# Optimization experiments

Hardware: AMD Instinct MI355X
Metric: run time of the kernel (lower is better)

The kernel has to match this reference:

```python
import jax, jax.numpy as jnp
import numpy as np

P = 2_000_000   # total gathered points (N1+N2+... after pillar grouping)
C_IN = 10       # mlps[0]: point feats + pillar-center offsets
C_OUT = 64      # mlps[1]
M = 200_000     # number of non-empty pillars (pillar_indices.shape[0])
BN_EPS = 1e-3


def setup_inputs() -> dict:
    key = jax.random.key(0)
    k0, k1, k2, k3, k4 = jax.random.split(key, 5)
    return {
        "group_features": jax.random.normal(k0, (P, C_IN), dtype=jnp.float32),
        "pillar_set_indices": jax.random.randint(k1, (P,), 0, M, dtype=jnp.int32),
        "num_pillars": M,
        # Linear(bias=False) weight, xavier-ish scale; stored (C_IN, C_OUT) so fwd is x @ W
        "W": jax.random.normal(k2, (C_IN, C_OUT), dtype=jnp.float32) * np.float32(1.0 / np.sqrt(C_IN)),
        "gamma": jnp.ones((C_OUT,), dtype=jnp.float32),
        "beta": jnp.zeros((C_OUT,), dtype=jnp.float32),
        "running_mean": jax.random.normal(k3, (C_OUT,), dtype=jnp.float32) * 0.1,
        "running_var": jax.random.uniform(k4, (C_OUT,), dtype=jnp.float32, minval=0.5, maxval=1.5),
    }


def reference(group_features, pillar_set_indices, num_pillars, W, gamma, beta, running_mean, running_var):
    # shared MLP: Linear(bias=False) -> BatchNorm1d(eval, eps=1e-3) -> ReLU
    h = group_features @ W                                   # (P, C_OUT)
    inv_std = gamma * jax.lax.rsqrt(running_var + BN_EPS)    # fold BN scale
    h = jax.nn.relu(h * inv_std + (beta - running_mean * inv_std))
    # scatter_max segment pooling into pillars; empty pillars -> 0 (ReLU output >= 0)
    pooled = jax.ops.segment_max(h, pillar_set_indices, num_segments=num_pillars)
    pillar_features = jnp.maximum(pooled, jnp.float32(0.0))  # (M, C_OUT)
    return pillar_features
```

## Files before the change

### kernel.cpp

```cpp
#include <hip/hip_runtime.h>


#define C_IN   10
#define C_OUT  64
#define BSHIFT 7
#define BPILL  128
#define MAXNBP 2048
#define NREG   8
#define SBLK   256
#define SCHUNK 2048
#define PPT    (SCHUNK / SBLK)
#define PBLK   512
#define SENT   (128u << 24)

typedef _Float16 half8 __attribute__((ext_vector_type(8)));
typedef float    f32x4 __attribute__((ext_vector_type(4)));

__global__ __launch_bounds__(SBLK)
void k_hist(const int* __restrict__ idx, int* __restrict__ tots,
            int P, int NBpad) {
    __shared__ int lh[MAXNBP];
    const int t = threadIdx.x;
    for (int b = t; b < NBpad; b += SBLK) lh[b] = 0;
    __syncthreads();
    const int base = blockIdx.x * SCHUNK;
#pragma unroll
    for (int i = 0; i < PPT; ++i) {
        int p = base + i * SBLK + t;
        if (p < P) atomicAdd(&lh[idx[p] >> BSHIFT], 1);
    }
    __syncthreads();
    int* row = tots + (size_t)(blockIdx.x & (NREG - 1)) * NBpad;
    for (int b = t; b < NBpad; b += SBLK) {
        int h = lh[b];
        if (h) atomicAdd(&row[b], h);
    }
}

__global__ __launch_bounds__(256)
void k_scan(const int* __restrict__ tots, int* __restrict__ starts,
            int* __restrict__ cursor, int E) {
    __shared__ int tmp[256];
    const int t = threadIdx.x;
    const int C = (E + 255) / 256;
    int my = 0;
    for (int j = 0; j < C; ++j) {
        int e = t * C + j;
        if (e < E) my += (tots[e] + 15) & ~15;
    }
    tmp[t] = my; __syncthreads();
#pragma unroll
    for (int off = 1; off < 256; off <<= 1) {
        int x = (t >= off) ? tmp[t - off] : 0;
        __syncthreads(); tmp[t] += x; __syncthreads();
    }
    int ex = tmp[t] - my;
    for (int j = 0; j < C; ++j) {
        int e = t * C + j;
        if (e < E) {
            starts[e] = ex; cursor[e] = ex;
            ex += (tots[e] + 15) & ~15;
        }
    }
    if (t == 255) starts[E] = ex;
}

__global__ __launch_bounds__(256)
void k_padfill(const int* __restrict__ tots, const int* __restrict__ starts,
               unsigned int* __restrict__ sorted, int E) {
    int e = blockIdx.x * 256 + threadIdx.x;
    if (e >= E) return;
    int s = starts[e] + tots[e];
    int e1 = starts[e + 1];
    for (int i = s; i < e1; ++i) sorted[i] = SENT;
}

__global__ __launch_bounds__(SBLK)
void k_split(const int* __restrict__ idx, int* __restrict__ cursor,
             unsigned int* __restrict__ sorted, int P, int NBpad) {
    __shared__ int lh[MAXNBP];
    __shared__ int rbase[MAXNBP];
    const int t = threadIdx.x;
    for (int b = t; b < NBpad; b += SBLK) lh[b] = 0;
    __syncthreads();
    const int base = blockIdx.x * SCHUNK;
    int mm[PPT];
#pragma unroll
    for (int i = 0; i < PPT; ++i) {
        int p = base + i * SBLK + t;
        mm[i] = (p < P) ? idx[p] : -1;
        if (mm[i] >= 0) atomicAdd(&lh[mm[i] >> BSHIFT], 1);
    }
    __syncthreads();
    int* crow = cursor + (size_t)(blockIdx.x & (NREG - 1)) * NBpad;
    for (int b = t; b < NBpad; b += SBLK) {
        int h = lh[b];
        rbase[b] = h ? atomicAdd(&crow[b], h) : 0;
        lh[b] = 0;
    }
    __syncthreads();
#pragma unroll
    for (int i = 0; i < PPT; ++i) {
        if (mm[i] >= 0) {
            int p = base + i * SBLK + t;
            int b = mm[i] >> BSHIFT;
            int slot = rbase[b] + atomicAdd(&lh[b], 1);
            sorted[slot] = (unsigned)p | ((unsigned)(mm[i] & (BPILL - 1)) << 24);
        }
    }
}

__global__ __launch_bounds__(PBLK, 8)
void k_pool(const float* __restrict__ gf,
            const unsigned int* __restrict__ sorted,
            const int* __restrict__ starts,
            const float* __restrict__ W,
            const float* __restrict__ gamma,
            const float* __restrict__ beta,
            const float* __restrict__ rmean,
            const float* __restrict__ rvar,
            float* __restrict__ out, int M, int NBpad) {
    __shared__ unsigned int acc[129 * 65];
    const int t = threadIdx.x;
    const int lane = t & 63;
    const int wv = t >> 6;
    const int n = lane & 15;
    const int q = lane >> 4;

    for (int i = t; i < 129 * 65; i += PBLK) acc[i] = 0u;

    half8 bfrag[4];
    float inv[4], bia[4];
#pragma unroll
    for (int tt = 0; tt < 4; ++tt) {
        int c = tt * 16 + n;
#pragma unroll
        for (int j = 0; j < 8; ++j) {
            int k = q * 8 + j;
            bfrag[tt][j] = (k < C_IN) ? (_Float16)W[k * C_OUT + c] : (_Float16)0.f;
        }
        float is = gamma[c] * rsqrtf(rvar[c] + 1e-3f);
        inv[tt] = is;
        bia[tt] = fmaf(-rmean[c], is, beta[c]);
    }
    __syncthreads();

    const int e  = wv * NBpad + blockIdx.x;
    const int s0 = starts[e];
    const int s1 = starts[e + 1];
    const float2* gf2 = (const float2*)gf;

    for (int rb = s0; rb < s1; rb += 64) {
        unsigned v = (rb + lane < s1) ? sorted[rb + lane] : SENT;
        const float2* src = gf2 + (size_t)(v & 0xFFFFFFu) * 5;
        float2 x0 = src[0], x1 = src[1], x2 = src[2], x3 = src[3], x4 = src[4];
        int u0 = __builtin_bit_cast(int, __builtin_amdgcn_cvt_pkrtz(x0.x, x0.y));
        int u1 = __builtin_bit_cast(int, __builtin_amdgcn_cvt_pkrtz(x1.x, x1.y));
        int u2 = __builtin_bit_cast(int, __builtin_amdgcn_cvt_pkrtz(x2.x, x2.y));
        int u3 = __builtin_bit_cast(int, __builtin_amdgcn_cvt_pkrtz(x3.x, x3.y));
        int u4 = __builtin_bit_cast(int, __builtin_amdgcn_cvt_pkrtz(x4.x, x4.y));

        const int ng = min(4, (s1 - rb) >> 4);
#pragma unroll
        for (int g = 0; g < 4; ++g) {
            if (g >= ng) break;
            const int sl = (g << 4) + n;
            int b0 = __shfl(u0, sl, 64);
            int b1 = __shfl(u1, sl, 64);
            int b2 = __shfl(u2, sl, 64);
            int b3 = __shfl(u3, sl, 64);
            int b4 = __shfl(u4, sl, 64);
            int4 a32;
            a32.x = (q == 0) ? b0 : ((q == 1) ? b4 : 0);
            a32.y = (q == 0) ? b1 : 0;
            a32.z = (q == 0) ? b2 : 0;
            a32.w = (q == 0) ? b3 : 0;
            half8 a = __builtin_bit_cast(half8, a32);
            f32x4 z = {0.f, 0.f, 0.f, 0.f};
            f32x4 d0 = __builtin_amdgcn_mfma_f32_16x16x32_f16(a, bfrag[0], z, 0, 0, 0);
            f32x4 d1 = __builtin_amdgcn_mfma_f32_16x16x32_f16(a, bfrag[1], z, 0, 0, 0);
            f32x4 d2 = __builtin_amdgcn_mfma_f32_16x16x32_f16(a, bfrag[2], z, 0, 0, 0);
            f32x4 d3 = __builtin_amdgcn_mfma_f32_16x16x32_f16(a, bfrag[3], z, 0, 0, 0);
#pragma unroll
            for (int r = 0; r < 4; ++r) {
                int pv = __shfl((int)v, (g << 4) + (q << 2) + r, 64);
                int abase = (int)(((unsigned)pv) >> 24) * 65 + n;
                float h0 = fmaxf(fmaf(d0[r], inv[0], bia[0]), 0.f);
                float h1 = fmaxf(fmaf(d1[r], inv[1], bia[1]), 0.f);
                float h2 = fmaxf(fmaf(d2[r], inv[2], bia[2]), 0.f);
                float h3 = fmaxf(fmaf(d3[r], inv[3], bia[3]), 0.f);
                atomicMax(&acc[abase +  0], __float_as_uint(h0));
                atomicMax(&acc[abase + 16], __float_as_uint(h1));
                atomicMax(&acc[abase + 32], __float_as_uint(h2));
                atomicMax(&acc[abase + 48], __float_as_uint(h3));
            }
        }
    }
    __syncthreads();

    const int mbase = blockIdx.x * BPILL;
#pragma unroll
    for (int i = 0; i < (BPILL * C_OUT) / PBLK; ++i) {
        int wdx = i * PBLK + t;
        int row = wdx >> 6, c = wdx & 63;
        int m = mbase + row;
        if (m < M) out[(size_t)m * C_OUT + c] = __uint_as_float(acc[row * 65 + c]);
    }
}

extern "C" void kernel_launch(void* const* d_in, const int* in_sizes, int n_in,
                              void* d_out, int out_size, void* d_ws, size_t ws_size,
                              hipStream_t stream) {
    const float* gf    = (const float*)d_in[0];
    const int*   idx   = (const int*)  d_in[1];
    const float* W     = (const float*)d_in[3];
    const float* gamma = (const float*)d_in[4];
    const float* beta  = (const float*)d_in[5];
    const float* rmean = (const float*)d_in[6];
    const float* rvar  = (const float*)d_in[7];
    float*       out   = (float*)d_out;

    const int P  = in_sizes[0] / C_IN;
    const int M  = out_size / C_OUT;
    const int NB    = (M + BPILL - 1) >> BSHIFT;
    const int NBpad = (NB + 32) & ~31;
    const int E     = NREG * NBpad;
    const int NSB   = (P + SCHUNK - 1) / SCHUNK;

    char* ws = (char*)d_ws;
    auto align256 = [](size_t x) { return (x + 255) & ~(size_t)255; };
    int* tots   = (int*)ws;  ws += align256((size_t)E * 4);
    int* starts = (int*)ws;  ws += align256((size_t)(E + 1) * 4);
    int* cursor = (int*)ws;  ws += align256((size_t)E * 4);
    unsigned int* sorted = (unsigned int*)ws;

    hipMemsetAsync(tots, 0, (size_t)E * 4, stream);
    k_hist   <<<NSB, SBLK, 0, stream>>>(idx, tots, P, NBpad);
    k_scan   <<<1,   256, 0, stream>>>(tots, starts, cursor, E);
    k_padfill<<<(E + 255) / 256, 256, 0, stream>>>(tots, starts, sorted, E);
    k_split  <<<NSB, SBLK, 0, stream>>>(idx, cursor, sorted, P, NBpad);
    k_pool   <<<NB,  PBLK, 0, stream>>>(gf, sorted, starts, W, gamma, beta,
                                        rmean, rvar, out, M, NBpad);
}
```

Measured before the change: 261.9 us.

## Fuse histogram, scan and scatter into one cooperative kernel; double-buffer pool loads

```diff
diff --git a/kernel.cpp b/kernel.cpp
--- a/kernel.cpp
+++ b/kernel.cpp
@@ -1,4 +1,5 @@
 #include <hip/hip_runtime.h>
+#include <hip/hip_cooperative_groups.h>
 
 
 #define C_IN   10
@@ -8,7 +9,7 @@
 #define MAXNBP 2048
 #define NREG   8
 #define SBLK   256
-#define SCHUNK 2048
+#define SCHUNK 4096
 #define PPT    (SCHUNK / SBLK)
 #define PBLK   512
 #define SENT   (128u << 24)
@@ -16,33 +17,40 @@
 typedef _Float16 half8 __attribute__((ext_vector_type(8)));
 typedef float    f32x4 __attribute__((ext_vector_type(4)));
 
-__global__ __launch_bounds__(SBLK)
-void k_hist(const int* __restrict__ idx, int* __restrict__ tots,
-            int P, int NBpad) {
+namespace cg = cooperative_groups;
+
+__global__ __launch_bounds__(SBLK, 4)
+void k_sort(const int* __restrict__ idx, int* __restrict__ tots,
+            int* __restrict__ starts, unsigned int* __restrict__ sorted,
+            int P, int NBpad, int E) {
     __shared__ int lh[MAXNBP];
-    const int t = threadIdx.x;
+    __shared__ int sbase[MAXNBP];
+    __shared__ int tmp[SBLK];
+    const int t  = threadIdx.x;
+    const int r0 = (blockIdx.x & (NREG - 1)) * NBpad;
+
     for (int b = t; b < NBpad; b += SBLK) lh[b] = 0;
     __syncthreads();
+
     const int base = blockIdx.x * SCHUNK;
+    int mm[PPT], rk[PPT];
 #pragma unroll
     for (int i = 0; i < PPT; ++i) {
         int p = base + i * SBLK + t;
-        if (p < P) atomicAdd(&lh[idx[p] >> BSHIFT], 1);
-    }
-    __syncthreads();
-    int* row = tots + (size_t)(blockIdx.x & (NREG - 1)) * NBpad;
+        mm[i] = (p < P) ? idx[p] : -1;
+        rk[i] = (mm[i] >= 0) ? atomicAdd(&lh[mm[i] >> BSHIFT], 1) : 0;
+    }
+    __syncthreads();
+
+    int* trow = tots + r0;
     for (int b = t; b < NBpad; b += SBLK) {
         int h = lh[b];
-        if (h) atomicAdd(&row[b], h);
-    }
-}
-
-__global__ __launch_bounds__(256)
-void k_scan(const int* __restrict__ tots, int* __restrict__ starts,
-            int* __restrict__ cursor, int E) {
-    __shared__ int tmp[256];
-    const int t = threadIdx.x;
-    const int C = (E + 255) / 256;
+        sbase[b] = h ? atomicAdd(&trow[b], h) : 0;
+    }
+
+    cg::this_grid().sync();
+
+    const int C = (E + SBLK - 1) / SBLK;
     int my = 0;
     for (int j = 0; j < C; ++j) {
         int e = t * C + j;
@@ -50,62 +58,31 @@
     }
     tmp[t] = my; __syncthreads();
 #pragma unroll
-    for (int off = 1; off < 256; off <<= 1) {
+    for (int off = 1; off < SBLK; off <<= 1) {
         int x = (t >= off) ? tmp[t - off] : 0;
         __syncthreads(); tmp[t] += x; __syncthreads();
     }
     int ex = tmp[t] - my;
+    const bool wr = (blockIdx.x == 0);
     for (int j = 0; j < C; ++j) {
         int e = t * C + j;
         if (e < E) {
-            starts[e] = ex; cursor[e] = ex;
+            if (wr) starts[e] = ex;
+            int d = e - r0;
+            if ((unsigned)d < (unsigned)NBpad) sbase[d] += ex;
             ex += (tots[e] + 15) & ~15;
         }
     }
-    if (t == 255) starts[E] = ex;
-}
-
-__global__ __launch_bounds__(256)
-void k_padfill(const int* __restrict__ tots, const int* __restrict__ starts,
-               unsigned int* __restrict__ sorted, int E) {
-    int e = blockIdx.x * 256 + threadIdx.x;
-    if (e >= E) return;
-    int s = starts[e] + tots[e];
-    int e1 = starts[e + 1];
-    for (int i = s; i < e1; ++i) sorted[i] = SENT;
-}
-
-__global__ __launch_bounds__(SBLK)
-void k_split(const int* __restrict__ idx, int* __restrict__ cursor,
-             unsigned int* __restrict__ sorted, int P, int NBpad) {
-    __shared__ int lh[MAXNBP];
-    __shared__ int rbase[MAXNBP];
-    const int t = threadIdx.x;
-    for (int b = t; b < NBpad; b += SBLK) lh[b] = 0;
-    __syncthreads();
-    const int base = blockIdx.x * SCHUNK;
-    int mm[PPT];
-#pragma unroll
-    for (int i = 0; i < PPT; ++i) {
-        int p = base + i * SBLK + t;
-        mm[i] = (p < P) ? idx[p] : -1;
-        if (mm[i] >= 0) atomicAdd(&lh[mm[i] >> BSHIFT], 1);
-    }
-    __syncthreads();
-    int* crow = cursor + (size_t)(blockIdx.x & (NREG - 1)) * NBpad;
-    for (int b = t; b < NBpad; b += SBLK) {
-        int h = lh[b];
-        rbase[b] = h ? atomicAdd(&crow[b], h) : 0;
-        lh[b] = 0;
-    }
-    __syncthreads();
+    if (wr && t == SBLK - 1) starts[E] = ex;
+    __syncthreads();
+
 #pragma unroll
     for (int i = 0; i < PPT; ++i) {
         if (mm[i] >= 0) {
             int p = base + i * SBLK + t;
             int b = mm[i] >> BSHIFT;
-            int slot = rbase[b] + atomicAdd(&lh[b], 1);
-            sorted[slot] = (unsigned)p | ((unsigned)(mm[i] & (BPILL - 1)) << 24);
+            sorted[sbase[b] + rk[i]] =
+                (unsigned)p | ((unsigned)(mm[i] & (BPILL - 1)) << 24);
         }
     }
 }
@@ -114,6 +91,7 @@
 void k_pool(const float* __restrict__ gf,
             const unsigned int* __restrict__ sorted,
             const int* __restrict__ starts,
+            const int* __restrict__ tots,
             const float* __restrict__ W,
             const float* __restrict__ gamma,
             const float* __restrict__ beta,
@@ -147,20 +125,10 @@
 
     const int e  = wv * NBpad + blockIdx.x;
     const int s0 = starts[e];
-    const int s1 = starts[e + 1];
+    const int s1 = s0 + tots[e];
     const float2* gf2 = (const float2*)gf;
 
-    for (int rb = s0; rb < s1; rb += 64) {
-        unsigned v = (rb + lane < s1) ? sorted[rb + lane] : SENT;
-        const float2* src = gf2 + (size_t)(v & 0xFFFFFFu) * 5;
-        float2 x0 = src[0], x1 = src[1], x2 = src[2], x3 = src[3], x4 = src[4];
-        int u0 = __builtin_bit_cast(int, __builtin_amdgcn_cvt_pkrtz(x0.x, x0.y));
-        int u1 = __builtin_bit_cast(int, __builtin_amdgcn_cvt_pkrtz(x1.x, x1.y));
-        int u2 = __builtin_bit_cast(int, __builtin_amdgcn_cvt_pkrtz(x2.x, x2.y));
-        int u3 = __builtin_bit_cast(int, __builtin_amdgcn_cvt_pkrtz(x3.x, x3.y));
-        int u4 = __builtin_bit_cast(int, __builtin_amdgcn_cvt_pkrtz(x4.x, x4.y));
-
-        const int ng = min(4, (s1 - rb) >> 4);
+    auto proc = [&](unsigned v, int u0, int u1, int u2, int u3, int u4, int ng) {
 #pragma unroll
         for (int g = 0; g < 4; ++g) {
             if (g >= ng) break;
@@ -195,6 +163,30 @@
                 atomicMax(&acc[abase + 48], __float_as_uint(h3));
             }
         }
+    };
+
+    for (int rb = s0; rb < s1; rb += 128) {
+        unsigned va = (rb + lane < s1) ? sorted[rb + lane] : SENT;
+        unsigned vb = (rb + 64 + lane < s1) ? sorted[rb + 64 + lane] : SENT;
+        const float2* sa = gf2 + (size_t)(va & 0xFFFFFFu) * 5;
+        const float2* sb = gf2 + (size_t)(vb & 0xFFFFFFu) * 5;
+        float2 xa0 = sa[0], xa1 = sa[1], xa2 = sa[2], xa3 = sa[3], xa4 = sa[4];
+        float2 xb0 = sb[0], xb1 = sb[1], xb2 = sb[2], xb3 = sb[3], xb4 = sb[4];
+        int uA0 = __builtin_bit_cast(int, __builtin_amdgcn_cvt_pkrtz(xa0.x, xa0.y));
+        int uA1 = __builtin_bit_cast(int, __builtin_amdgcn_cvt_pkrtz(xa1.x, xa1.y));
+        int uA2 = __builtin_bit_cast(int, __builtin_amdgcn_cvt_pkrtz(xa2.x, xa2.y));
+        int uA3 = __builtin_bit_cast(int, __builtin_amdgcn_cvt_pkrtz(xa3.x, xa3.y));
+        int uA4 = __builtin_bit_cast(int, __builtin_amdgcn_cvt_pkrtz(xa4.x, xa4.y));
+        int uB0 = __builtin_bit_cast(int, __builtin_amdgcn_cvt_pkrtz(xb0.x, xb0.y));
+        int uB1 = __builtin_bit_cast(int, __builtin_amdgcn_cvt_pkrtz(xb1.x, xb1.y));
+        int uB2 = __builtin_bit_cast(int, __builtin_amdgcn_cvt_pkrtz(xb2.x, xb2.y));
+        int uB3 = __builtin_bit_cast(int, __builtin_amdgcn_cvt_pkrtz(xb3.x, xb3.y));
+        int uB4 = __builtin_bit_cast(int, __builtin_amdgcn_cvt_pkrtz(xb4.x, xb4.y));
+        __builtin_amdgcn_sched_barrier(0);
+
+        proc(va, uA0, uA1, uA2, uA3, uA4, min(4, ((s1 - rb) + 15) >> 4));
+        if (rb + 64 < s1)
+            proc(vb, uB0, uB1, uB2, uB3, uB4, min(4, ((s1 - rb - 64) + 15) >> 4));
     }
     __syncthreads();
 
@@ -231,14 +223,16 @@
     auto align256 = [](size_t x) { return (x + 255) & ~(size_t)255; };
     int* tots   = (int*)ws;  ws += align256((size_t)E * 4);
     int* starts = (int*)ws;  ws += align256((size_t)(E + 1) * 4);
-    int* cursor = (int*)ws;  ws += align256((size_t)E * 4);
     unsigned int* sorted = (unsigned int*)ws;
 
     hipMemsetAsync(tots, 0, (size_t)E * 4, stream);
-    k_hist   <<<NSB, SBLK, 0, stream>>>(idx, tots, P, NBpad);
-    k_scan   <<<1,   256, 0, stream>>>(tots, starts, cursor, E);
-    k_padfill<<<(E + 255) / 256, 256, 0, stream>>>(tots, starts, sorted, E);
-    k_split  <<<NSB, SBLK, 0, stream>>>(idx, cursor, sorted, P, NBpad);
-    k_pool   <<<NB,  PBLK, 0, stream>>>(gf, sorted, starts, W, gamma, beta,
-                                        rmean, rvar, out, M, NBpad);
+
+    int Pv = P, NBpadv = NBpad, Ev = E;
+    void* kargs[] = { (void*)&idx, (void*)&tots, (void*)&starts, (void*)&sorted,
+                      (void*)&Pv, (void*)&NBpadv, (void*)&Ev };
+    hipLaunchCooperativeKernel((void*)k_sort, dim3(NSB), dim3(SBLK),
+                               kargs, 0, stream);
+
+    k_pool<<<NB, PBLK, 0, stream>>>(gf, sorted, starts, tots, W, gamma, beta,
+                                    rmean, rvar, out, M, NBpad);
 }
```

Result: slower. 370.2 us (+41.3%).

## Fuse scan into split kernel, drop padfill, and use persistent pool blocks

Applied to the files above, without the earlier changes.

```diff
diff --git a/kernel.cpp b/kernel.cpp
--- a/kernel.cpp
+++ b/kernel.cpp
@@ -37,12 +37,30 @@
     }
 }
 
-__global__ __launch_bounds__(256)
-void k_scan(const int* __restrict__ tots, int* __restrict__ starts,
-            int* __restrict__ cursor, int E) {
-    __shared__ int tmp[256];
-    const int t = threadIdx.x;
-    const int C = (E + 255) / 256;
+__global__ __launch_bounds__(SBLK)
+void k_split(const int* __restrict__ idx, const int* __restrict__ tots,
+             int* __restrict__ cursor, int* __restrict__ starts,
+             unsigned int* __restrict__ sorted, int P, int NBpad, int E) {
+    __shared__ int lh[MAXNBP];
+    __shared__ int sbase[MAXNBP];
+    __shared__ int tmp[SBLK];
+    const int t  = threadIdx.x;
+    const int r0 = (blockIdx.x & (NREG - 1)) * NBpad;
+
+    for (int b = t; b < NBpad; b += SBLK) lh[b] = 0;
+    __syncthreads();
+
+    const int base = blockIdx.x * SCHUNK;
+    int mm[PPT], rk[PPT];
+#pragma unroll
+    for (int i = 0; i < PPT; ++i) {
+        int p = base + i * SBLK + t;
+        mm[i] = (p < P) ? idx[p] : -1;
+        rk[i] = (mm[i] >= 0) ? atomicAdd(&lh[mm[i] >> BSHIFT], 1) : 0;
+    }
+    __syncthreads();
+
+    const int C = (E + SBLK - 1) / SBLK;
     int my = 0;
     for (int j = 0; j < C; ++j) {
         int e = t * C + j;
@@ -50,62 +68,37 @@
     }
     tmp[t] = my; __syncthreads();
 #pragma unroll
-    for (int off = 1; off < 256; off <<= 1) {
+    for (int off = 1; off < SBLK; off <<= 1) {
         int x = (t >= off) ? tmp[t - off] : 0;
         __syncthreads(); tmp[t] += x; __syncthreads();
     }
     int ex = tmp[t] - my;
+    const bool wr = (blockIdx.x == 0);
     for (int j = 0; j < C; ++j) {
         int e = t * C + j;
         if (e < E) {
-            starts[e] = ex; cursor[e] = ex;
+            if (wr) starts[e] = ex;
+            int d = e - r0;
+            if ((unsigned)d < (unsigned)NBpad) sbase[d] = ex;
             ex += (tots[e] + 15) & ~15;
         }
     }
-    if (t == 255) starts[E] = ex;
-}
-
-__global__ __launch_bounds__(256)
-void k_padfill(const int* __restrict__ tots, const int* __restrict__ starts,
-               unsigned int* __restrict__ sorted, int E) {
-    int e = blockIdx.x * 256 + threadIdx.x;
-    if (e >= E) return;
-    int s = starts[e] + tots[e];
-    int e1 = starts[e + 1];
-    for (int i = s; i < e1; ++i) sorted[i] = SENT;
-}
-
-__global__ __launch_bounds__(SBLK)
-void k_split(const int* __restrict__ idx, int* __restrict__ cursor,
-             unsigned int* __restrict__ sorted, int P, int NBpad) {
-    __shared__ int lh[MAXNBP];
-    __shared__ int rbase[MAXNBP];
-    const int t = threadIdx.x;
-    for (int b = t; b < NBpad; b += SBLK) lh[b] = 0;
-    __syncthreads();
-    const int base = blockIdx.x * SCHUNK;
-    int mm[PPT];
-#pragma unroll
-    for (int i = 0; i < PPT; ++i) {
-        int p = base + i * SBLK + t;
-        mm[i] = (p < P) ? idx[p] : -1;
-        if (mm[i] >= 0) atomicAdd(&lh[mm[i] >> BSHIFT], 1);
-    }
-    __syncthreads();
-    int* crow = cursor + (size_t)(blockIdx.x & (NREG - 1)) * NBpad;
+    if (wr && t == SBLK - 1) starts[E] = ex;
+    __syncthreads();
+
     for (int b = t; b < NBpad; b += SBLK) {
         int h = lh[b];
-        rbase[b] = h ? atomicAdd(&crow[b], h) : 0;
-        lh[b] = 0;
-    }
-    __syncthreads();
+        if (h) sbase[b] += atomicAdd(&cursor[r0 + b], h);
+    }
+    __syncthreads();
+
 #pragma unroll
     for (int i = 0; i < PPT; ++i) {
         if (mm[i] >= 0) {
             int p = base + i * SBLK + t;
             int b = mm[i] >> BSHIFT;
-            int slot = rbase[b] + atomicAdd(&lh[b], 1);
-            sorted[slot] = (unsigned)p | ((unsigned)(mm[i] & (BPILL - 1)) << 24);
+            sorted[sbase[b] + rk[i]] =
+                (unsigned)p | ((unsigned)(mm[i] & (BPILL - 1)) << 24);
         }
     }
 }
@@ -114,21 +107,22 @@
 void k_pool(const float* __restrict__ gf,
             const unsigned int* __restrict__ sorted,
             const int* __restrict__ starts,
+            const int* __restrict__ tots,
+            int* __restrict__ ctr,
             const float* __restrict__ W,
             const float* __restrict__ gamma,
             const float* __restrict__ beta,
             const float* __restrict__ rmean,
             const float* __restrict__ rvar,
-            float* __restrict__ out, int M, int NBpad) {
+            float* __restrict__ out, int M, int NB, int NBpad) {
     __shared__ unsigned int acc[129 * 65];
+    __shared__ int sblk;
     const int t = threadIdx.x;
     const int lane = t & 63;
     const int wv = t >> 6;
     const int n = lane & 15;
     const int q = lane >> 4;
 
-    for (int i = t; i < 129 * 65; i += PBLK) acc[i] = 0u;
-
     half8 bfrag[4];
     float inv[4], bia[4];
 #pragma unroll
@@ -143,68 +137,77 @@
         inv[tt] = is;
         bia[tt] = fmaf(-rmean[c], is, beta[c]);
     }
-    __syncthreads();
-
-    const int e  = wv * NBpad + blockIdx.x;
-    const int s0 = starts[e];
-    const int s1 = starts[e + 1];
+
     const float2* gf2 = (const float2*)gf;
 
-    for (int rb = s0; rb < s1; rb += 64) {
-        unsigned v = (rb + lane < s1) ? sorted[rb + lane] : SENT;
-        const float2* src = gf2 + (size_t)(v & 0xFFFFFFu) * 5;
-        float2 x0 = src[0], x1 = src[1], x2 = src[2], x3 = src[3], x4 = src[4];
-        int u0 = __builtin_bit_cast(int, __builtin_amdgcn_cvt_pkrtz(x0.x, x0.y));
-        int u1 = __builtin_bit_cast(int, __builtin_amdgcn_cvt_pkrtz(x1.x, x1.y));
-        int u2 = __builtin_bit_cast(int, __builtin_amdgcn_cvt_pkrtz(x2.x, x2.y));
-        int u3 = __builtin_bit_cast(int, __builtin_amdgcn_cvt_pkrtz(x3.x, x3.y));
-        int u4 = __builtin_bit_cast(int, __builtin_amdgcn_cvt_pkrtz(x4.x, x4.y));
-
-        const int ng = min(4, (s1 - rb) >> 4);
-#pragma unroll
-        for (int g = 0; g < 4; ++g) {
-            if (g >= ng) break;
-            const int sl = (g << 4) + n;
-            int b0 = __shfl(u0, sl, 64);
-            int b1 = __shfl(u1, sl, 64);
-            int b2 = __shfl(u2, sl, 64);
-            int b3 = __shfl(u3, sl, 64);
-            int b4 = __shfl(u4, sl, 64);
-            int4 a32;
-            a32.x = (q == 0) ? b0 : ((q == 1) ? b4 : 0);
-            a32.y = (q == 0) ? b1 : 0;
-            a32.z = (q == 0) ? b2 : 0;
-            a32.w = (q == 0) ? b3 : 0;
-            half8 a = __builtin_bit_cast(half8, a32);
-            f32x4 z = {0.f, 0.f, 0.f, 0.f};
-            f32x4 d0 = __builtin_amdgcn_mfma_f32_16x16x32_f16(a, bfrag[0], z, 0, 0, 0);
-            f32x4 d1 = __builtin_amdgcn_mfma_f32_16x16x32_f16(a, bfrag[1], z, 0, 0, 0);
-            f32x4 d2 = __builtin_amdgcn_mfma_f32_16x16x32_f16(a, bfrag[2], z, 0, 0, 0);
-            f32x4 d3 = __builtin_amdgcn_mfma_f32_16x16x32_f16(a, bfrag[3], z, 0, 0, 0);
-#pragma unroll
-            for (int r = 0; r < 4; ++r) {
-                int pv = __shfl((int)v, (g << 4) + (q << 2) + r, 64);
-                int abase = (int)(((unsigned)pv) >> 24) * 65 + n;
-                float h0 = fmaxf(fmaf(d0[r], inv[0], bia[0]), 0.f);
-                float h1 = fmaxf(fmaf(d1[r], inv[1], bia[1]), 0.f);
-                float h2 = fmaxf(fmaf(d2[r], inv[2], bia[2]), 0.f);
-                float h3 = fmaxf(fmaf(d3[r], inv[3], bia[3]), 0.f);
-                atomicMax(&acc[abase +  0], __float_as_uint(h0));
-                atomicMax(&acc[abase + 16], __float_as_uint(h1));
-                atomicMax(&acc[abase + 32], __float_as_uint(h2));
-                atomicMax(&acc[abase + 48], __float_as_uint(h3));
+    for (;;) {
+        __syncthreads();
+        if (t == 0) sblk = atomicAdd(ctr, 1);
+        for (int i = t; i < 129 * 65; i += PBLK) acc[i] = 0u;
+        __syncthreads();
+        const int blk = sblk;
+        if (blk >= NB) break;
+
+        const int e  = wv * NBpad + blk;
+        const int s0 = starts[e];
+        const int s1 = s0 + tots[e];
+
+        for (int rb = s0; rb < s1; rb += 64) {
+            unsigned v = (rb + lane < s1) ? sorted[rb + lane] : SENT;
+            const float2* src = gf2 + (size_t)(v & 0xFFFFFFu) * 5;
+            float2 x0 = src[0], x1 = src[1], x2 = src[2], x3 = src[3], x4 = src[4];
+            int u0 = __builtin_bit_cast(int, __builtin_amdgcn_cvt_pkrtz(x0.x, x0.y));
+            int u1 = __builtin_bit_cast(int, __builtin_amdgcn_cvt_pkrtz(x1.x, x1.y));
+            int u2 = __builtin_bit_cast(int, __builtin_amdgcn_cvt_pkrtz(x2.x, x2.y));
+            int u3 = __builtin_bit_cast(int, __builtin_amdgcn_cvt_pkrtz(x3.x, x3.y));
+            int u4 = __builtin_bit_cast(int, __builtin_amdgcn_cvt_pkrtz(x4.x, x4.y));
+
+            const int ng = min(4, ((s1 - rb) + 15) >> 4);
+#pragma unroll
+            for (int g = 0; g < 4; ++g) {
+                if (g >= ng) break;
+                const int sl = (g << 4) + n;
+                int b0 = __shfl(u0, sl, 64);
+                int b1 = __shfl(u1, sl, 64);
+                int b2 = __shfl(u2, sl, 64);
+                int b3 = __shfl(u3, sl, 64);
+                int b4 = __shfl(u4, sl, 64);
+                int4 a32;
+                a32.x = (q == 0) ? b0 : ((q == 1) ? b4 : 0);
+                a32.y = (q == 0) ? b1 : 0;
+                a32.z = (q == 0) ? b2 : 0;
+                a32.w = (q == 0) ? b3 : 0;
+                half8 a = __builtin_bit_cast(half8, a32);
+                f32x4 z = {0.f, 0.f, 0.f, 0.f};
+                f32x4 d0 = __builtin_amdgcn_mfma_f32_16x16x32_f16(a, bfrag[0], z, 0, 0, 0);
+                f32x4 d1 = __builtin_amdgcn_mfma_f32_16x16x32_f16(a, bfrag[1], z, 0, 0, 0);
+                f32x4 d2 = __builtin_amdgcn_mfma_f32_16x16x32_f16(a, bfrag[2], z, 0, 0, 0);
+                f32x4 d3 = __builtin_amdgcn_mfma_f32_16x16x32_f16(a, bfrag[3], z, 0, 0, 0);
+#pragma unroll
+                for (int r = 0; r < 4; ++r) {
+                    int pv = __shfl((int)v, (g << 4) + (q << 2) + r, 64);
+                    int abase = (int)(((unsigned)pv) >> 24) * 65 + n;
+                    float h0 = fmaxf(fmaf(d0[r], inv[0], bia[0]), 0.f);
+                    float h1 = fmaxf(fmaf(d1[r], inv[1], bia[1]), 0.f);
+                    float h2 = fmaxf(fmaf(d2[r], inv[2], bia[2]), 0.f);
+                    float h3 = fmaxf(fmaf(d3[r], inv[3], bia[3]), 0.f);
+                    atomicMax(&acc[abase +  0], __float_as_uint(h0));
+                    atomicMax(&acc[abase + 16], __float_as_uint(h1));
+                    atomicMax(&acc[abase + 32], __float_as_uint(h2));
+                    atomicMax(&acc[abase + 48], __float_as_uint(h3));
+                }
             }
         }
-    }
-    __syncthreads();
-
-    const int mbase = blockIdx.x * BPILL;
-#pragma unroll
-    for (int i = 0; i < (BPILL * C_OUT) / PBLK; ++i) {
-        int wdx = i * PBLK + t;
-        int row = wdx >> 6, c = wdx & 63;
-        int m = mbase + row;
-        if (m < M) out[(size_t)m * C_OUT + c] = __uint_as_float(acc[row * 65 + c]);
+        __syncthreads();
+
+        const int mbase = blk * BPILL;
+#pragma unroll
+        for (int i = 0; i < (BPILL * C_OUT) / PBLK; ++i) {
+            int wdx = i * PBLK + t;
+            int row = wdx >> 6, c = wdx & 63;
+            int m = mbase + row;
+            if (m < M) out[(size_t)m * C_OUT + c] = __uint_as_float(acc[row * 65 + c]);
+        }
     }
 }
 
@@ -230,15 +233,18 @@
     char* ws = (char*)d_ws;
     auto align256 = [](size_t x) { return (x + 255) & ~(size_t)255; };
     int* tots   = (int*)ws;  ws += align256((size_t)E * 4);
+    int* cursor = (int*)ws;  ws += align256((size_t)E * 4);
+    int* ctr    = (int*)ws;  ws += 256;
     int* starts = (int*)ws;  ws += align256((size_t)(E + 1) * 4);
-    int* cursor = (int*)ws;  ws += align256((size_t)E * 4);
     unsigned int* sorted = (unsigned int*)ws;
 
-    hipMemsetAsync(tots, 0, (size_t)E * 4, stream);
-    k_hist   <<<NSB, SBLK, 0, stream>>>(idx, tots, P, NBpad);
-    k_scan   <<<1,   256, 0, stream>>>(tots, starts, cursor, E);
-    k_padfill<<<(E + 255) / 256, 256, 0, stream>>>(tots, starts, sorted, E);
-    k_split  <<<NSB, SBLK, 0, stream>>>(idx, cursor, sorted, P, NBpad);
-    k_pool   <<<NB,  PBLK, 0, stream>>>(gf, sorted, starts, W, gamma, beta,
-                                        rmean, rvar, out, M, NBpad);
-}
+    hipMemsetAsync(tots, 0, (size_t)((char*)starts - (char*)tots), stream);
+
+    k_hist <<<NSB, SBLK, 0, stream>>>(idx, tots, P, NBpad);
+    k_split<<<NSB, SBLK, 0, stream>>>(idx, tots, cursor, starts, sorted,
+                                      P, NBpad, E);
+
+    const int NPB = NB < 1024 ? NB : 1024;
+    k_pool <<<NPB, PBLK, 0, stream>>>(gf, sorted, starts, tots, ctr, W, gamma,
+                                      beta, rmean, rvar, out, M, NB, NBpad);
+}
```

Measured after the change: 282.9 us. 1.08x slower.
